# Kernel tuning notes

Hardware: AMD Instinct MI355X
Metric: run time of the kernel (lower is better)

Reference implementation:

```python
import jax, jax.numpy as jnp
import numpy as np

NH = 8
D_MODEL = 512
D_K = D_MODEL // NH
B, S = 2, 4096


def setup_inputs() -> dict:
    key = jax.random.key(0)
    ks = jax.random.split(key, 8)
    scale = 1.0 / np.sqrt(D_MODEL)
    return {
        "query": jax.random.normal(ks[0], (B, S, D_MODEL), dtype=jnp.float32),
        "key": jax.random.normal(ks[1], (B, S, D_MODEL), dtype=jnp.float32),
        "value": jax.random.normal(ks[2], (B, S, D_MODEL), dtype=jnp.float32),
        "mask": jax.random.randint(ks[3], (B, 1, S, S), 0, 2) > 0,
        "Wq": jax.random.normal(ks[4], (D_MODEL, D_MODEL), dtype=jnp.float32) * scale,
        "Wk": jax.random.normal(ks[5], (D_MODEL, D_MODEL), dtype=jnp.float32) * scale,
        "Wv": jax.random.normal(ks[6], (D_MODEL, D_MODEL), dtype=jnp.float32) * scale,
        "Wo": jax.random.normal(ks[7], (D_MODEL, D_MODEL), dtype=jnp.float32) * scale,
    }


def reference(query, key, value, mask, Wq, Wk, Wv, Wo):
    # Linear (no bias): torch Linear stores W as [out, in], y = x @ W^T.
    def proj(x, W):
        # [B, S, D] -> [B, nh, S, d_k]
        y = jnp.einsum("bsd,ed->bse", x, W)
        return y.reshape(B, S, NH, D_K).transpose(0, 2, 1, 3)

    q = proj(query, Wq)
    k = proj(key, Wk)
    v = proj(value, Wv)

    scores = jnp.einsum("bhqd,bhkd->bhqk", q, k) / jnp.sqrt(jnp.float32(D_K))
    scores = jnp.where(mask, jnp.float32(-1e9), scores)
    p_attn = jax.nn.softmax(scores, axis=-1)
    x = jnp.einsum("bhqk,bhkd->bhqd", p_attn, v)  # [B, nh, S, d_k]
    x = x.transpose(0, 2, 1, 3).reshape(B, S, D_MODEL)
    return jnp.einsum("bsd,ed->bse", x, Wo)
```

## Files before the change

### kernel.cpp

```cpp
#include <hip/hip_runtime.h>


#define S_LEN   4096
#define DM      512
#define NHEAD   8
#define DKH     64
#define NT      (S_LEN / 64)
#define LOG2E   1.44269504088896f
#define NEG2    (-1.44269504e9f)
#define MINIT   (-3.402823466e38f)
#define QSCALE  (0.125f * LOG2E)

typedef __bf16 bf16x8 __attribute__((ext_vector_type(8)));
typedef __bf16 bf16x4 __attribute__((ext_vector_type(4)));
typedef float  f32x4  __attribute__((ext_vector_type(4)));
typedef unsigned long long u64;

#define F3(a,b,c) fmaxf(fmaxf((a),(b)),(c))

__device__ inline float exp2fast(float x) {
    float r;
    asm("v_exp_f32 %0, %1" : "=v"(r) : "v"(x));
    return r;
}
__device__ inline unsigned cvtpk(float lo, float hi) {
    unsigned r;
    asm("v_cvt_pk_bf16_f32 %0, %1, %2" : "=v"(r) : "v"(lo), "v"(hi));
    return r;
}

__device__ inline void gload_lds16(const void* g, void* l) {
    __builtin_amdgcn_global_load_lds(
        (const __attribute__((address_space(1))) unsigned int*)g,
        (__attribute__((address_space(3))) unsigned int*)l, 16, 0, 0);
}

__device__ inline uint4 cvt8(float4 a, float4 b) {
    union { bf16x8 v; uint4 u; } c;
    c.v[0] = (__bf16)a.x; c.v[1] = (__bf16)a.y;
    c.v[2] = (__bf16)a.z; c.v[3] = (__bf16)a.w;
    c.v[4] = (__bf16)b.x; c.v[5] = (__bf16)b.y;
    c.v[6] = (__bf16)b.z; c.v[7] = (__bf16)b.w;
    return c.u;
}

__global__ __launch_bounds__(256)
void prep(const float* __restrict__ q, const float* __restrict__ k,
          const float* __restrict__ v, const int* __restrict__ mask,
          const float* __restrict__ Wq, const float* __restrict__ Wk,
          const float* __restrict__ Wv, const float* __restrict__ Wo,
          __bf16* __restrict__ wb, __bf16* __restrict__ xb,
          u64* __restrict__ bits)
{
    __shared__ u64 sm[4][64];
    const int blk = blockIdx.x, tid = threadIdx.x;

    if (blk < 512) {
        const int t = blk * 256 + tid;
        const int e = t * 8, z = e >> 18, i = e & 262143;
        const float* W = (z == 0) ? Wq : (z == 1) ? Wk : (z == 2) ? Wv : Wo;
        const float4 a = *(const float4*)&W[i];
        const float4 b = *(const float4*)&W[i + 4];
        *(uint4*)&wb[e] = cvt8(a, b);
    } else if (blk < 6656) {
        const int t = (blk - 512) * 256 + tid;
        const int e = t * 8, z = e >> 22, i = e & 4194303;
        const float* X = (z == 0) ? q : (z == 1) ? k : v;
        const float4 a = *(const float4*)&X[i];
        const float4 b = *(const float4*)&X[i + 4];
        *(uint4*)&xb[e] = cvt8(a, b);
    } else {
        const int w4 = tid >> 6, lane = tid & 63;
        const int gw = (blk - 6656) * 4 + w4;
        const int p  = gw >> 6;
        const int r0 = (gw & 63) << 6;
        const int bb = p >> 6, wc = p & 63;
        #pragma unroll 4
        for (int it = 0; it < 64; ++it) {
            const int r = r0 + it;
            const size_t idx = (((size_t)(bb * S_LEN + r)) << 12) + (wc << 6) + lane;
            const u64 bal = __ballot(mask[idx] != 0);
            if (lane == 0) sm[w4][it] = bal;
        }
        bits[((size_t)p << 12) + r0 + lane] = sm[w4][lane];
    }
}

template<int MODE>
__global__ __launch_bounds__(512, 4)
void gemm_mfma(const __bf16* __restrict__ X0, const __bf16* __restrict__ X1,
               const __bf16* __restrict__ X2, const __bf16* __restrict__ Wb,
               __bf16* __restrict__ Y0, __bf16* __restrict__ Y1,
               __bf16* __restrict__ Y2, float* __restrict__ Yf)
{
    __shared__ __align__(16) char lds[65536];

    const int tid  = threadIdx.x;
    const int lane = tid & 63;
    const int l15  = lane & 15;
    const int lhi  = lane >> 4;
    const int w    = tid >> 6;
    const int wr   = w >> 2;
    const int wc   = w & 3;
    const int row0 = blockIdx.x << 7;
    const int col0 = blockIdx.y << 7;
    const int z    = blockIdx.z;

    const __bf16* X = (z == 0) ? X0 : (z == 1) ? X1 : X2;
    const __bf16* W = Wb + (size_t)(MODE == 0 ? z : 3) * DM * DM;

    f32x4 acc[4][2];
    #pragma unroll
    for (int m = 0; m < 4; ++m)
        #pragma unroll
        for (int n = 0; n < 2; ++n)
            acc[m][n] = (f32x4){0.f, 0.f, 0.f, 0.f};

    auto stage = [&](int c, int k0) {
        char* Xs = lds + c * 32768;
        char* Ws = Xs + 16384;
        #pragma unroll
        for (int s = 0; s < 2; ++s) {
            const int f = w * 128 + s * 64 + lane;
            const int r = f >> 3, sl = f & 7;
            const size_t go = (size_t)r * DM + k0 + ((sl ^ (r & 7)) << 3);
            gload_lds16(&X[(size_t)row0 * DM + go], Xs + w * 2048 + s * 1024);
            gload_lds16(&W[(size_t)col0 * DM + go], Ws + w * 2048 + s * 1024);
        }
    };

    stage(0, 0);
    __syncthreads();

    for (int t = 0; t < 8; ++t) {
        const int c = t & 1;
        if (t < 7) stage(c ^ 1, (t + 1) * 64);

        const char* Xs = lds + c * 32768;
        const char* Ws = Xs + 16384;
        #pragma unroll
        for (int kk = 0; kk < 2; ++kk) {
            bf16x8 xf[4], wf[2];
            #pragma unroll
            for (int m = 0; m < 4; ++m) {
                const int r = wr * 64 + m * 16 + l15;
                xf[m] = *(const bf16x8*)(Xs + r * 128 + ((((kk << 2) + lhi) ^ (r & 7)) << 4));
            }
            #pragma unroll
            for (int n = 0; n < 2; ++n) {
                const int r = wc * 32 + n * 16 + l15;
                wf[n] = *(const bf16x8*)(Ws + r * 128 + ((((kk << 2) + lhi) ^ (r & 7)) << 4));
            }
            __builtin_amdgcn_s_setprio(1);
            #pragma unroll
            for (int m = 0; m < 4; ++m)
                #pragma unroll
                for (int n = 0; n < 2; ++n)
                    acc[m][n] = __builtin_amdgcn_mfma_f32_16x16x32_bf16(wf[n], xf[m], acc[m][n], 0, 0, 0);
            __builtin_amdgcn_s_setprio(0);
        }
        __syncthreads();
    }

    const float osc = (MODE == 0 && z == 0) ? QSCALE : 1.0f;
    #pragma unroll
    for (int m = 0; m < 4; ++m) {
        const int r = row0 + wr * 64 + m * 16 + l15;
        #pragma unroll
        for (int n = 0; n < 2; ++n) {
            const int cb = col0 + wc * 32 + n * 16 + lhi * 4;
            if (MODE == 0) {
                bf16x4 o4;
                o4[0] = (__bf16)(acc[m][n][0] * osc);
                o4[1] = (__bf16)(acc[m][n][1] * osc);
                o4[2] = (__bf16)(acc[m][n][2] * osc);
                o4[3] = (__bf16)(acc[m][n][3] * osc);
                const int bb = r >> 12, srow = r & 4095;
                const int hh = cb >> 6, dk = cb & 63;
                __bf16* Yb = (z == 0) ? Y0 : (z == 1) ? Y1 : Y2;
                *(bf16x4*)&Yb[(((size_t)(bb * NHEAD + hh)) * S_LEN + srow) * DKH + dk] = o4;
            } else {
                *(float4*)&Yf[(size_t)r * DM + cb] = *(float4*)&acc[m][n];
            }
        }
    }
}

__global__ __launch_bounds__(512, 4)
void attn_mfma(const __bf16* __restrict__ Q, const __bf16* __restrict__ K,
               const __bf16* __restrict__ V, const u64* __restrict__ bits,
               __bf16* __restrict__ ctx)
{
    __shared__ __align__(16) char lds[49152];

    const int tid  = threadIdx.x;
    const int lane = tid & 63;
    const int w    = tid >> 6;
    const int l15  = lane & 15;
    const int lhi  = lane >> 4;
    const int q0   = blockIdx.x << 7;
    const int h    = blockIdx.y;
    const int b    = blockIdx.z;

    const __bf16* Qb = Q + (size_t)(b * NHEAD + h) * S_LEN * DKH;
    const __bf16* Kb = K + (size_t)(b * NHEAD + h) * S_LEN * DKH;
    const __bf16* Vb = V + (size_t)(b * NHEAD + h) * S_LEN * DKH;

    const int qrow = q0 + w * 16 + l15;
    const u64* Mb = bits + ((size_t)b << 18) + qrow;

    const bf16x8 qa0 = *(const bf16x8*)&Qb[(size_t)qrow * DKH + lhi * 8];
    const bf16x8 qa1 = *(const bf16x8*)&Qb[(size_t)qrow * DKH + 32 + lhi * 8];

    char* psb = lds + 32768 + w * 2048;

    f32x4 o[4];
    float m_r = MINIT, l_r = 0.f;
    #pragma unroll
    for (int dt = 0; dt < 4; ++dt) o[dt] = (f32x4){0.f, 0.f, 0.f, 0.f};

    const int krow = tid >> 3, kslot = tid & 7;
    const int vj   = tid & 63, vd0 = (tid >> 6) * 8;

    gload_lds16(&Kb[(size_t)krow * DKH + ((kslot ^ (krow & 7)) << 3)],
                lds + w * 1024);
    {
        const uint4 v0 = *(const uint4*)&Vb[(size_t)vj * DKH + vd0];
        char* Vt = lds + 8192;
        const __bf16* vr = (const __bf16*)&v0;
        #pragma unroll
        for (int i = 0; i < 8; ++i) {
            const int dd = vd0 + i;
            *(__bf16*)(Vt + ((dd * 128 + vj * 2) ^ ((dd & 7) << 4))) = vr[i];
        }
    }
    u64 mcur = Mb[0];
    __syncthreads();

    for (int t = 0; t < NT; ++t) {
        const int c  = t & 1;
        const int tn = (t + 1 < NT) ? (t + 1) : t;

        gload_lds16(&Kb[(size_t)((tn << 6) + krow) * DKH + ((kslot ^ (krow & 7)) << 3)],
                    lds + (c ^ 1) * 16384 + w * 1024);
        const uint4 vnxt = *(const uint4*)&Vb[(size_t)((tn << 6) + vj) * DKH + vd0];
        const u64   mnxt = Mb[(size_t)tn << 12];

        const char* Ksb = lds + c * 16384;
        const char* Vtb = Ksb + 8192;

        f32x4 s[4];
        __builtin_amdgcn_s_setprio(1);
        #pragma unroll
        for (int tt = 0; tt < 4; ++tt) {
            const int kr  = tt * 16 + l15;
            const int off = kr * 128 + ((lhi ^ (kr & 7)) << 4);
            const bf16x8 kb0 = *(const bf16x8*)(Ksb + off);
            const bf16x8 kb1 = *(const bf16x8*)(Ksb + (off ^ 64));
            f32x4 zz = (f32x4){0.f, 0.f, 0.f, 0.f};
            zz    = __builtin_amdgcn_mfma_f32_16x16x32_bf16(kb0, qa0, zz, 0, 0, 0);
            s[tt] = __builtin_amdgcn_mfma_f32_16x16x32_bf16(kb1, qa1, zz, 0, 0, 0);
        }
        __builtin_amdgcn_s_setprio(0);

        const unsigned int lo = (unsigned int)mcur, hi = (unsigned int)(mcur >> 32);
        unsigned int shf[4];
        shf[0] = lo >> (lhi << 2);
        shf[1] = lo >> (16 + (lhi << 2));
        shf[2] = hi >> (lhi << 2);
        shf[3] = hi >> (16 + (lhi << 2));

        float pv[4][4];
        #pragma unroll
        for (int tt = 0; tt < 4; ++tt)
            #pragma unroll
            for (int r = 0; r < 4; ++r)
                pv[tt][r] = ((shf[tt] >> r) & 1) ? NEG2 : s[tt][r];

        float a0 = F3(pv[0][0], pv[0][1], pv[0][2]);
        float a1 = F3(pv[0][3], pv[1][0], pv[1][1]);
        float a2 = F3(pv[1][2], pv[1][3], pv[2][0]);
        float a3 = F3(pv[2][1], pv[2][2], pv[2][3]);
        float a4 = F3(pv[3][0], pv[3][1], pv[3][2]);
        float tmax = fmaxf(F3(a0, a1, a2), F3(a3, a4, pv[3][3]));
        tmax = fmaxf(tmax, __shfl_xor(tmax, 16));
        tmax = fmaxf(tmax, __shfl_xor(tmax, 32));

        if (!__all(tmax <= m_r + 8.f)) {
            const float newm  = fmaxf(m_r, tmax);
            const float alpha = exp2fast(m_r - newm);
            m_r = newm;
            l_r *= alpha;
            #pragma unroll
            for (int dt = 0; dt < 4; ++dt) {
                o[dt][0] *= alpha; o[dt][1] *= alpha;
                o[dt][2] *= alpha; o[dt][3] *= alpha;
            }
        }

        float rsum = 0.f;
        #pragma unroll
        for (int tt = 0; tt < 4; ++tt)
            #pragma unroll
            for (int r = 0; r < 4; ++r) {
                pv[tt][r] = exp2fast(pv[tt][r] - m_r);
                rsum += pv[tt][r];
            }
        rsum += __shfl_xor(rsum, 16);
        rsum += __shfl_xor(rsum, 32);
        l_r += rsum;

        #pragma unroll
        for (int tt = 0; tt < 4; ++tt) {
            uint2 pk;
            pk.x = cvtpk(pv[tt][0], pv[tt][1]);
            pk.y = cvtpk(pv[tt][2], pv[tt][3]);
            const int off = l15 * 128
                          + ((((tt << 1) + (lhi >> 1)) ^ (l15 & 7)) << 4)
                          + ((lhi & 1) << 3);
            *(uint2*)(psb + off) = pk;
        }
        const int poff = l15 * 128 + ((lhi ^ (l15 & 7)) << 4);
        const bf16x8 pb0 = *(const bf16x8*)(psb + poff);
        const bf16x8 pb1 = *(const bf16x8*)(psb + (poff ^ 64));

        __builtin_amdgcn_s_setprio(1);
        #pragma unroll
        for (int dt = 0; dt < 4; ++dt) {
            const int vrow = dt * 16 + l15;
            const int voff = vrow * 128 + ((lhi ^ (vrow & 7)) << 4);
            const bf16x8 vb0 = *(const bf16x8*)(Vtb + voff);
            const bf16x8 vb1 = *(const bf16x8*)(Vtb + (voff ^ 64));
            o[dt] = __builtin_amdgcn_mfma_f32_16x16x32_bf16(vb0, pb0, o[dt], 0, 0, 0);
            o[dt] = __builtin_amdgcn_mfma_f32_16x16x32_bf16(vb1, pb1, o[dt], 0, 0, 0);
        }
        __builtin_amdgcn_s_setprio(0);

        {
            char* Vt = lds + (c ^ 1) * 16384 + 8192;
            const __bf16* vr = (const __bf16*)&vnxt;
            #pragma unroll
            for (int i = 0; i < 8; ++i) {
                const int dd = vd0 + i;
                *(__bf16*)(Vt + ((dd * 128 + vj * 2) ^ ((dd & 7) << 4))) = vr[i];
            }
        }
        __syncthreads();
        mcur = mnxt;
    }

    const float inv = 1.f / l_r;
    #pragma unroll
    for (int dt = 0; dt < 4; ++dt) {
        bf16x4 ov;
        ov[0] = (__bf16)(o[dt][0] * inv);
        ov[1] = (__bf16)(o[dt][1] * inv);
        ov[2] = (__bf16)(o[dt][2] * inv);
        ov[3] = (__bf16)(o[dt][3] * inv);
        *(bf16x4*)&ctx[((size_t)b * S_LEN + qrow) * DM + h * DKH + dt * 16 + lhi * 4] = ov;
    }
}

extern "C" void kernel_launch(void* const* d_in, const int* in_sizes, int n_in,
                              void* d_out, int out_size, void* d_ws, size_t ws_size,
                              hipStream_t stream)
{
    const float* q    = (const float*)d_in[0];
    const float* k    = (const float*)d_in[1];
    const float* v    = (const float*)d_in[2];
    const int*   mask = (const int*)d_in[3];
    const float* Wq   = (const float*)d_in[4];
    const float* Wk   = (const float*)d_in[5];
    const float* Wv   = (const float*)d_in[6];
    const float* Wo   = (const float*)d_in[7];
    float* out = (float*)d_out;

    const size_t per = (size_t)2 * S_LEN * DM;
    __bf16* wb   = (__bf16*)d_ws;
    __bf16* xb   = wb + (size_t)4 * DM * DM;
    __bf16* Qh   = xb + 3 * per;
    __bf16* Kh   = Qh + per;
    __bf16* Vh   = Kh + per;
    __bf16* ctx  = Vh + per;
    u64*    bits = (u64*)(ctx + per);

    prep<<<dim3(8704), dim3(256), 0, stream>>>(q, k, v, mask,
                                               Wq, Wk, Wv, Wo, wb, xb, bits);

    gemm_mfma<0><<<dim3(64, 4, 3), dim3(512), 0, stream>>>(
        xb, xb + per, xb + 2 * per, wb, Qh, Kh, Vh, nullptr);

    attn_mfma<<<dim3(32, 8, 2), dim3(512), 0, stream>>>(Qh, Kh, Vh, bits, ctx);

    gemm_mfma<1><<<dim3(64, 4, 1), dim3(512), 0, stream>>>(
        ctx, ctx, ctx, wb, nullptr, nullptr, nullptr, out);
}
```

Measured before the change: 402.2 us.

## Fuse fp32-to-bf16 input conversion into projection GEMM and halve attention block size

Result: slower. 422.2 us (+5.0%).

```diff
diff --git a/kernel.cpp b/kernel.cpp
--- a/kernel.cpp
+++ b/kernel.cpp
@@ -36,21 +36,17 @@
 }
 
 __device__ inline uint4 cvt8(float4 a, float4 b) {
-    union { bf16x8 v; uint4 u; } c;
-    c.v[0] = (__bf16)a.x; c.v[1] = (__bf16)a.y;
-    c.v[2] = (__bf16)a.z; c.v[3] = (__bf16)a.w;
-    c.v[4] = (__bf16)b.x; c.v[5] = (__bf16)b.y;
-    c.v[6] = (__bf16)b.z; c.v[7] = (__bf16)b.w;
-    return c.u;
+    uint4 u;
+    u.x = cvtpk(a.x, a.y); u.y = cvtpk(a.z, a.w);
+    u.z = cvtpk(b.x, b.y); u.w = cvtpk(b.z, b.w);
+    return u;
 }
 
 __global__ __launch_bounds__(256)
-void prep(const float* __restrict__ q, const float* __restrict__ k,
-          const float* __restrict__ v, const int* __restrict__ mask,
+void prep(const int* __restrict__ mask,
           const float* __restrict__ Wq, const float* __restrict__ Wk,
           const float* __restrict__ Wv, const float* __restrict__ Wo,
-          __bf16* __restrict__ wb, __bf16* __restrict__ xb,
-          u64* __restrict__ bits)
+          __bf16* __restrict__ wb, u64* __restrict__ bits)
 {
     __shared__ u64 sm[4][64];
     const int blk = blockIdx.x, tid = threadIdx.x;
@@ -62,16 +58,9 @@
         const float4 a = *(const float4*)&W[i];
         const float4 b = *(const float4*)&W[i + 4];
         *(uint4*)&wb[e] = cvt8(a, b);
-    } else if (blk < 6656) {
-        const int t = (blk - 512) * 256 + tid;
-        const int e = t * 8, z = e >> 22, i = e & 4194303;
-        const float* X = (z == 0) ? q : (z == 1) ? k : v;
-        const float4 a = *(const float4*)&X[i];
-        const float4 b = *(const float4*)&X[i + 4];
-        *(uint4*)&xb[e] = cvt8(a, b);
     } else {
         const int w4 = tid >> 6, lane = tid & 63;
-        const int gw = (blk - 6656) * 4 + w4;
+        const int gw = (blk - 512) * 4 + w4;
         const int p  = gw >> 6;
         const int r0 = (gw & 63) << 6;
         const int bb = p >> 6, wc = p & 63;
@@ -88,8 +77,9 @@
 
 template<int MODE>
 __global__ __launch_bounds__(512, 4)
-void gemm_mfma(const __bf16* __restrict__ X0, const __bf16* __restrict__ X1,
-               const __bf16* __restrict__ X2, const __bf16* __restrict__ Wb,
+void gemm_mfma(const float* __restrict__ X0, const float* __restrict__ X1,
+               const float* __restrict__ X2, const __bf16* __restrict__ Xb,
+               const __bf16* __restrict__ Wb,
                __bf16* __restrict__ Y0, __bf16* __restrict__ Y1,
                __bf16* __restrict__ Y2, float* __restrict__ Yf)
 {
@@ -106,8 +96,11 @@
     const int col0 = blockIdx.y << 7;
     const int z    = blockIdx.z;
 
-    const __bf16* X = (z == 0) ? X0 : (z == 1) ? X1 : X2;
-    const __bf16* W = Wb + (size_t)(MODE == 0 ? z : 3) * DM * DM;
+    const float*  Xf = (z == 0) ? X0 : (z == 1) ? X1 : X2;
+    const __bf16* W  = Wb + (size_t)(MODE == 0 ? z : 3) * DM * DM;
+
+    const int sr = tid >> 2;
+    const int sc = (tid & 3) << 1;
 
     f32x4 acc[4][2];
     #pragma unroll
@@ -116,7 +109,7 @@
         for (int n = 0; n < 2; ++n)
             acc[m][n] = (f32x4){0.f, 0.f, 0.f, 0.f};
 
-    auto stage = [&](int c, int k0) {
+    auto wstage = [&](int c, int k0) {
         char* Xs = lds + c * 32768;
         char* Ws = Xs + 16384;
         #pragma unroll
@@ -124,17 +117,36 @@
             const int f = w * 128 + s * 64 + lane;
             const int r = f >> 3, sl = f & 7;
             const size_t go = (size_t)r * DM + k0 + ((sl ^ (r & 7)) << 3);
-            gload_lds16(&X[(size_t)row0 * DM + go], Xs + w * 2048 + s * 1024);
+            if (MODE == 1)
+                gload_lds16(&Xb[(size_t)row0 * DM + go], Xs + w * 2048 + s * 1024);
             gload_lds16(&W[(size_t)col0 * DM + go], Ws + w * 2048 + s * 1024);
         }
     };
 
-    stage(0, 0);
+    float4 xr0, xr1, xr2, xr3;
+    auto xload = [&](int k0) {
+        const size_t base = (size_t)(row0 + sr) * DM + k0 + sc * 8;
+        xr0 = *(const float4*)&Xf[base];
+        xr1 = *(const float4*)&Xf[base + 4];
+        xr2 = *(const float4*)&Xf[base + 8];
+        xr3 = *(const float4*)&Xf[base + 12];
+    };
+    auto xwrite = [&](int c) {
+        char* Xs = lds + c * 32768;
+        *(uint4*)(Xs + sr * 128 + ((sc       ^ (sr & 7)) << 4)) = cvt8(xr0, xr1);
+        *(uint4*)(Xs + sr * 128 + (((sc + 1) ^ (sr & 7)) << 4)) = cvt8(xr2, xr3);
+    };
+
+    wstage(0, 0);
+    if (MODE == 0) { xload(0); xwrite(0); }
     __syncthreads();
 
     for (int t = 0; t < 8; ++t) {
         const int c = t & 1;
-        if (t < 7) stage(c ^ 1, (t + 1) * 64);
+        if (t < 7) {
+            wstage(c ^ 1, (t + 1) * 64);
+            if (MODE == 0) xload((t + 1) * 64);
+        }
 
         const char* Xs = lds + c * 32768;
         const char* Ws = Xs + 16384;
@@ -159,6 +171,7 @@
                     acc[m][n] = __builtin_amdgcn_mfma_f32_16x16x32_bf16(wf[n], xf[m], acc[m][n], 0, 0, 0);
             __builtin_amdgcn_s_setprio(0);
         }
+        if (MODE == 0 && t < 7) xwrite(c ^ 1);
         __syncthreads();
     }
 
@@ -186,19 +199,19 @@
     }
 }
 
-__global__ __launch_bounds__(512, 4)
+__global__ __launch_bounds__(256, 4)
 void attn_mfma(const __bf16* __restrict__ Q, const __bf16* __restrict__ K,
                const __bf16* __restrict__ V, const u64* __restrict__ bits,
                __bf16* __restrict__ ctx)
 {
-    __shared__ __align__(16) char lds[49152];
+    __shared__ __align__(16) char lds[40960];
 
     const int tid  = threadIdx.x;
     const int lane = tid & 63;
     const int w    = tid >> 6;
     const int l15  = lane & 15;
     const int lhi  = lane >> 4;
-    const int q0   = blockIdx.x << 7;
+    const int q0   = blockIdx.x << 6;
     const int h    = blockIdx.y;
     const int b    = blockIdx.z;
 
@@ -219,21 +232,31 @@
     #pragma unroll
     for (int dt = 0; dt < 4; ++dt) o[dt] = (f32x4){0.f, 0.f, 0.f, 0.f};
 
-    const int krow = tid >> 3, kslot = tid & 7;
-    const int vj   = tid & 63, vd0 = (tid >> 6) * 8;
-
-    gload_lds16(&Kb[(size_t)krow * DKH + ((kslot ^ (krow & 7)) << 3)],
-                lds + w * 1024);
-    {
-        const uint4 v0 = *(const uint4*)&Vb[(size_t)vj * DKH + vd0];
-        char* Vt = lds + 8192;
-        const __bf16* vr = (const __bf16*)&v0;
+    const int kr0 = tid >> 3, ks0 = tid & 7;
+    const int kr1 = kr0 + 32, ks1 = ks0;
+    const int vj = tid & 63, vd0 = (tid >> 6) * 8;
+
+    auto kstage = [&](int c, int j0) {
+        gload_lds16(&Kb[(size_t)(j0 + kr0) * DKH + ((ks0 ^ (kr0 & 7)) << 3)],
+                    lds + c * 16384 + w * 1024);
+        gload_lds16(&Kb[(size_t)(j0 + kr1) * DKH + ((ks1 ^ (kr1 & 7)) << 3)],
+                    lds + c * 16384 + 4096 + w * 1024);
+    };
+    auto vwrite = [&](int c, uint4 va, uint4 vb2) {
+        char* Vt = lds + c * 16384 + 8192;
+        const __bf16* ra = (const __bf16*)&va;
+        const __bf16* rb = (const __bf16*)&vb2;
         #pragma unroll
         for (int i = 0; i < 8; ++i) {
-            const int dd = vd0 + i;
-            *(__bf16*)(Vt + ((dd * 128 + vj * 2) ^ ((dd & 7) << 4))) = vr[i];
-        }
-    }
+            const int d1 = vd0 + i, d2 = vd0 + 32 + i;
+            *(__bf16*)(Vt + ((d1 * 128 + vj * 2) ^ ((d1 & 7) << 4))) = ra[i];
+            *(__bf16*)(Vt + ((d2 * 128 + vj * 2) ^ ((d2 & 7) << 4))) = rb[i];
+        }
+    };
+
+    kstage(0, 0);
+    vwrite(0, *(const uint4*)&Vb[(size_t)vj * DKH + vd0],
+              *(const uint4*)&Vb[(size_t)vj * DKH + vd0 + 32]);
     u64 mcur = Mb[0];
     __syncthreads();
 
@@ -241,9 +264,9 @@
         const int c  = t & 1;
         const int tn = (t + 1 < NT) ? (t + 1) : t;
 
-        gload_lds16(&Kb[(size_t)((tn << 6) + krow) * DKH + ((kslot ^ (krow & 7)) << 3)],
-                    lds + (c ^ 1) * 16384 + w * 1024);
-        const uint4 vnxt = *(const uint4*)&Vb[(size_t)((tn << 6) + vj) * DKH + vd0];
+        kstage(c ^ 1, tn << 6);
+        const uint4 vna = *(const uint4*)&Vb[(size_t)((tn << 6) + vj) * DKH + vd0];
+        const uint4 vnb = *(const uint4*)&Vb[(size_t)((tn << 6) + vj) * DKH + vd0 + 32];
         const u64   mnxt = Mb[(size_t)tn << 12];
 
         const char* Ksb = lds + c * 16384;
@@ -336,15 +359,7 @@
         }
         __builtin_amdgcn_s_setprio(0);
 
-        {
-            char* Vt = lds + (c ^ 1) * 16384 + 8192;
-            const __bf16* vr = (const __bf16*)&vnxt;
-            #pragma unroll
-            for (int i = 0; i < 8; ++i) {
-                const int dd = vd0 + i;
-                *(__bf16*)(Vt + ((dd * 128 + vj * 2) ^ ((dd & 7) << 4))) = vr[i];
-            }
-        }
+        vwrite(c ^ 1, vna, vnb);
         __syncthreads();
         mcur = mnxt;
     }
@@ -377,21 +392,19 @@
 
     const size_t per = (size_t)2 * S_LEN * DM;
     __bf16* wb   = (__bf16*)d_ws;
-    __bf16* xb   = wb + (size_t)4 * DM * DM;
-    __bf16* Qh   = xb + 3 * per;
+    __bf16* Qh   = wb + (size_t)4 * DM * DM;
     __bf16* Kh   = Qh + per;
     __bf16* Vh   = Kh + per;
     __bf16* ctx  = Vh + per;
     u64*    bits = (u64*)(ctx + per);
 
-    prep<<<dim3(8704), dim3(256), 0, stream>>>(q, k, v, mask,
-                                               Wq, Wk, Wv, Wo, wb, xb, bits);
+    prep<<<dim3(2560), dim3(256), 0, stream>>>(mask, Wq, Wk, Wv, Wo, wb, bits);
 
     gemm_mfma<0><<<dim3(64, 4, 3), dim3(512), 0, stream>>>(
-        xb, xb + per, xb + 2 * per, wb, Qh, Kh, Vh, nullptr);
-
-    attn_mfma<<<dim3(32, 8, 2), dim3(512), 0, stream>>>(Qh, Kh, Vh, bits, ctx);
+        q, k, v, nullptr, wb, Qh, Kh, Vh, nullptr);
+
+    attn_mfma<<<dim3(64, 8, 2), dim3(256), 0, stream>>>(Qh, Kh, Vh, bits, ctx);
 
     gemm_mfma<1><<<dim3(64, 4, 1), dim3(512), 0, stream>>>(
-        ctx, ctx, ctx, wb, nullptr, nullptr, nullptr, out);
-}
+        nullptr, nullptr, nullptr, ctx, wb, nullptr, nullptr, nullptr, out);
+}
```
